# Performance work log

Hardware: AMD Instinct MI355X
Metric: run time of the kernel (lower is better)

## Reference

```python
import jax, jax.numpy as jnp
import numpy as np

MAX_ITER = 20
F_TOL = 1e-6
FREE_NUM = 64  # free_idx[1] + 1
TRUNC = (0, 512)  # truncate_idx


def setup_inputs() -> dict:
    key = jax.random.key(0)
    ks = jax.random.split(key, 8)
    bsz, in_dim, hid, out_dim, m = 1024, 512, 1024, 256, 128
    return {
        "b_primal": jax.random.normal(ks[0], (bsz, in_dim), jnp.float32),
        "W0": jax.random.normal(ks[1], (hid, in_dim), jnp.float32) / np.sqrt(in_dim).astype(np.float32),
        "b0": jnp.zeros((hid,), jnp.float32),
        "W1": jax.random.normal(ks[2], (hid, hid), jnp.float32) / np.sqrt(hid).astype(np.float32),
        "b1": jnp.zeros((hid,), jnp.float32),
        "W2": jax.random.normal(ks[3], (out_dim, hid), jnp.float32) / np.sqrt(hid).astype(np.float32),
        "b2": jnp.zeros((out_dim,), jnp.float32),
        "A": jax.random.normal(ks[4], (m, out_dim), jnp.float32) * 0.1,
        "b_vec": jax.random.normal(ks[5], (m,), jnp.float32),
        # scaled so spectral norm < 1 -> contracting fixed-point iteration
        "WzProj": jax.random.normal(ks[6], (out_dim, out_dim), jnp.float32) * 0.03,
        "WbProj": jax.random.normal(ks[7], (out_dim, m), jnp.float32) * 0.1,
    }


def reference(b_primal, W0, b0, W1, b1, W2, b2, A, b_vec, WzProj, WbProj):
    # eval-mode forward of DualNN (report_projection=True)
    x = b_primal[:, TRUNC[0]:TRUNC[1]]
    h = jax.nn.relu(x @ W0.T + b0)
    h = jax.nn.relu(h @ W1.T + b1)
    out = h @ W2.T + b2                      # [bsz, output_dim]

    bias_proj = b_vec @ WbProj.T             # [output_dim]

    def cond(state):
        _, it, res = state
        return (it <= MAX_ITER) & (res > F_TOL)

    def body(state):
        z, it, _ = state
        z = bias_proj + z @ WzProj.T         # affine projection step
        u = z[:, :FREE_NUM]
        v = jax.nn.relu(z[:, FREE_NUM:])     # clamp non-free coordinates
        z = jnp.concatenate([u, v], axis=-1)
        res = jnp.max(jnp.abs(z @ A.T - b_vec))  # inf-norm equality residual
        return z, it + 1, res

    z_star, curr_iter, _ = jax.lax.while_loop(
        cond, body, (out, jnp.int32(1), jnp.float32(jnp.inf)))
    return (z_star, out, curr_iter)
```

## Files before the change

kernel.cpp:

```cpp
#include <hip/hip_runtime.h>

typedef __attribute__((ext_vector_type(8))) __bf16 bf16x8;
typedef __attribute__((ext_vector_type(4))) float f32x4;

#define MAX_ITER_N 20
#define F_TOL_F 1e-6f
#define FREE_NUM_N 64

#define BSZ 1024
#define IN_DIM 512
#define HID 1024
#define OUT_DIM 256
#define M_CON 128

#define WS_BAR   0
#define WS_RES   8
#define WS_BP    48
#define WS_H1    304
#define WS_H2    (WS_H1 + 524288)
#define WS_W2C   (WS_H2 + 524288)
#define WS_WZG   (WS_W2C + 131072)
#define WS_AG    (WS_WZG + 32768)

__device__ __forceinline__ unsigned short f2bf(float f) {
    unsigned int u = __float_as_uint(f);
    u += 0x7fffu + ((u >> 16) & 1u);
    return (unsigned short)(u >> 16);
}

__device__ __forceinline__ uint4 cvt8(float4 a, float4 b) {
    union { unsigned short s[8]; uint4 v; } u;
    u.s[0] = f2bf(a.x); u.s[1] = f2bf(a.y); u.s[2] = f2bf(a.z); u.s[3] = f2bf(a.w);
    u.s[4] = f2bf(b.x); u.s[5] = f2bf(b.y); u.s[6] = f2bf(b.z); u.s[7] = f2bf(b.w);
    return u.v;
}

__device__ __forceinline__ void gload_lds16(const unsigned short* g, unsigned short* l) {
    __builtin_amdgcn_global_load_lds(
        (const __attribute__((address_space(1))) unsigned int*)(const void*)g,
        (__attribute__((address_space(3))) unsigned int*)(void*)l, 16, 0, 0);
}

__device__ __forceinline__ bf16x8 ldfrag(const unsigned short* p) {
    return __builtin_bit_cast(bf16x8, *(const uint4*)p);
}

__device__ __forceinline__ bf16x8 frag128(const unsigned short* lds, int row, int gc) {
    int phys = gc ^ (row & 15);
    return __builtin_bit_cast(bf16x8, *(const uint4*)(lds + row * 128 + phys * 8));
}

__device__ __forceinline__ void grid_barrier(unsigned int* bar, unsigned int nblk) {
    __syncthreads();
    if (threadIdx.x == 0) {
        unsigned int g = __hip_atomic_load(&bar[1], __ATOMIC_RELAXED, __HIP_MEMORY_SCOPE_AGENT);
        unsigned int a = __hip_atomic_fetch_add(&bar[0], 1u, __ATOMIC_ACQ_REL, __HIP_MEMORY_SCOPE_AGENT);
        if (a == nblk - 1u) {
            __hip_atomic_store(&bar[0], 0u, __ATOMIC_RELAXED, __HIP_MEMORY_SCOPE_AGENT);
            __hip_atomic_store(&bar[1], g + 1u, __ATOMIC_RELEASE, __HIP_MEMORY_SCOPE_AGENT);
        } else {
            while (__hip_atomic_load(&bar[1], __ATOMIC_ACQUIRE, __HIP_MEMORY_SCOPE_AGENT) == g)
                __builtin_amdgcn_s_sleep(2);
        }
    }
    __syncthreads();
}

template<int K, int NTN, bool AF32, bool BF32, bool RELU>
__device__ __forceinline__ void gemm32_dev(
    const void* __restrict__ Av, const void* __restrict__ Bv,
    const float* __restrict__ bias, unsigned short* __restrict__ C, int N_,
    int tile, unsigned short (*As)[32 * 128], unsigned short (*Bs)[32 * 128])
{
    constexpr int NCH = K / 128;
    const int tid = threadIdx.x;
    const int w = tid >> 6;
    const int lane = tid & 63;
    const int ln = lane & 15;
    const int q  = lane >> 4;
    const int wr = w >> 1;
    const int wc = w & 1;
    const int row0 = (tile / NTN) * 32;
    const int col0 = (tile % NTN) * 32;

    int goff[2], lgran[2], soff[2], dbase[2];
#pragma unroll
    for (int i = 0; i < 2; ++i) {
        int P = i * 256 + tid;
        int row = P >> 4, gc = P & 15;
        goff[i]  = row * K + gc * 8;
        lgran[i] = row * 128 + (gc ^ (row & 15)) * 8;
        int base = w * 128 + i * 64;
        int P2 = base + lane;
        int row2 = P2 >> 4, pgc = P2 & 15;
        soff[i]  = row2 * K + (pgc ^ (row2 & 15)) * 8;
        dbase[i] = base * 8;
    }

    const float* Af = (const float*)Av + row0 * K;
    const float* Bf = (const float*)Bv + col0 * K;
    const unsigned short* Ah = (const unsigned short*)Av + row0 * K;
    const unsigned short* Bh = (const unsigned short*)Bv + col0 * K;

    float4 fa[2][2], fb[2][2];
    if constexpr (AF32) {
#pragma unroll
        for (int i = 0; i < 2; ++i) {
            fa[i][0] = *(const float4*)(Af + goff[i]);
            fa[i][1] = *(const float4*)(Af + goff[i] + 4);
        }
#pragma unroll
        for (int i = 0; i < 2; ++i) *(uint4*)&As[0][lgran[i]] = cvt8(fa[i][0], fa[i][1]);
    } else {
#pragma unroll
        for (int i = 0; i < 2; ++i) gload_lds16(Ah + soff[i], &As[0][dbase[i]]);
    }
    if constexpr (BF32) {
#pragma unroll
        for (int i = 0; i < 2; ++i) {
            fb[i][0] = *(const float4*)(Bf + goff[i]);
            fb[i][1] = *(const float4*)(Bf + goff[i] + 4);
        }
#pragma unroll
        for (int i = 0; i < 2; ++i) *(uint4*)&Bs[0][lgran[i]] = cvt8(fb[i][0], fb[i][1]);
    } else {
#pragma unroll
        for (int i = 0; i < 2; ++i) gload_lds16(Bh + soff[i], &Bs[0][dbase[i]]);
    }

    f32x4 acc = {0.f, 0.f, 0.f, 0.f};

    for (int c = 0; c < NCH; ++c) {
        __syncthreads();
        const int nb = (c + 1) & 1;
        if (c + 1 < NCH) {
            if constexpr (AF32) {
#pragma unroll
                for (int i = 0; i < 2; ++i) {
                    fa[i][0] = *(const float4*)(Af + (c + 1) * 128 + goff[i]);
                    fa[i][1] = *(const float4*)(Af + (c + 1) * 128 + goff[i] + 4);
                }
            } else {
#pragma unroll
                for (int i = 0; i < 2; ++i)
                    gload_lds16(Ah + (c + 1) * 128 + soff[i], &As[nb][dbase[i]]);
            }
            if constexpr (BF32) {
#pragma unroll
                for (int i = 0; i < 2; ++i) {
                    fb[i][0] = *(const float4*)(Bf + (c + 1) * 128 + goff[i]);
                    fb[i][1] = *(const float4*)(Bf + (c + 1) * 128 + goff[i] + 4);
                }
            } else {
#pragma unroll
                for (int i = 0; i < 2; ++i)
                    gload_lds16(Bh + (c + 1) * 128 + soff[i], &Bs[nb][dbase[i]]);
            }
        }
        const unsigned short* Ac = As[c & 1];
        const unsigned short* Bc = Bs[c & 1];
#pragma unroll
        for (int ks = 0; ks < 4; ++ks) {
            bf16x8 af = frag128(Ac, wr * 16 + ln, ks * 4 + q);
            bf16x8 bf = frag128(Bc, wc * 16 + ln, ks * 4 + q);
            acc = __builtin_amdgcn_mfma_f32_16x16x32_bf16(af, bf, acc, 0, 0, 0);
        }
        if (c + 1 < NCH) {
            if constexpr (AF32) {
#pragma unroll
                for (int i = 0; i < 2; ++i) *(uint4*)&As[nb][lgran[i]] = cvt8(fa[i][0], fa[i][1]);
            }
            if constexpr (BF32) {
#pragma unroll
                for (int i = 0; i < 2; ++i) *(uint4*)&Bs[nb][lgran[i]] = cvt8(fb[i][0], fb[i][1]);
            }
        }
    }

    const int cc = col0 + wc * 16 + ln;
    const float bv = bias[cc];
#pragma unroll
    for (int i = 0; i < 4; ++i) {
        int r = row0 + wr * 16 + q * 4 + i;
        float v = acc[i] + bv;
        if (RELU) v = fmaxf(v, 0.0f);
        C[r * N_ + cc] = f2bf(v);
    }
}

__global__ __launch_bounds__(256, 4) void g1_k(
    const float* __restrict__ b_primal, const float* __restrict__ W0,
    const float* __restrict__ b0, float* __restrict__ ws)
{
    __shared__ __align__(16) unsigned short As[2][32 * 128];
    __shared__ __align__(16) unsigned short Bs[2][32 * 128];
    if (blockIdx.x == 0 && threadIdx.x < 40)
        ((unsigned int*)ws)[threadIdx.x] = 0u;
    unsigned short* h1c = (unsigned short*)(ws + WS_H1);
    gemm32_dev<IN_DIM, 32, true, true, true>(b_primal, W0, b0, h1c, HID,
                                             blockIdx.x, As, Bs);
}

__global__ __launch_bounds__(256, 4) void g2_k(
    const float* __restrict__ W1, const float* __restrict__ b1,
    const float* __restrict__ W2, const float* __restrict__ Wz,
    const float* __restrict__ Amat, const float* __restrict__ b_vec,
    const float* __restrict__ WbProj, float* __restrict__ ws)
{
    __shared__ __align__(16) unsigned short As[2][32 * 128];
    __shared__ __align__(16) unsigned short Bs[2][32 * 128];
    const int tid = threadIdx.x;
    if (blockIdx.x >= 1024) {
        int b = blockIdx.x - 1024;
        if (b == 352) {
            float s = 0.0f;
            const float* wrow = WbProj + tid * M_CON;
            for (int k = 0; k < M_CON; ++k) s += b_vec[k] * wrow[k];
            (ws + WS_BP)[tid] = s;
            return;
        }
        const float* src; unsigned short* dst; int off;
        if (b < 256)      { src = W2;   dst = (unsigned short*)(ws + WS_W2C); off = b; }
        else if (b < 320) { src = Wz;   dst = (unsigned short*)(ws + WS_WZG); off = b - 256; }
        else              { src = Amat; dst = (unsigned short*)(ws + WS_AG);  off = b - 320; }
        int idx = off * 1024 + tid * 4;
        float4 v = *(const float4*)(src + idx);
        ushort4 o;
        o.x = f2bf(v.x); o.y = f2bf(v.y); o.z = f2bf(v.z); o.w = f2bf(v.w);
        *(ushort4*)(dst + idx) = o;
        return;
    }
    const unsigned short* h1c = (const unsigned short*)(ws + WS_H1);
    unsigned short* h2c = (unsigned short*)(ws + WS_H2);
    gemm32_dev<HID, 32, false, true, true>(h1c, W1, b1, h2c, HID,
                                           blockIdx.x, As, Bs);
}

__global__ __launch_bounds__(256, 1) void loop_k(
    const float* __restrict__ b2, const float* __restrict__ b_vec,
    const float* __restrict__ WzProj, float* __restrict__ out,
    float* __restrict__ ws)
{
    __shared__ __align__(16) unsigned char smem[16 * 257 * 4 + 64];
    unsigned int* bar = (unsigned int*)(ws + WS_BAR);
    unsigned int* res = (unsigned int*)(ws + WS_RES);
    const float* bp = ws + WS_BP;
    const unsigned short* h2c = (const unsigned short*)(ws + WS_H2);
    const unsigned short* W2c = (const unsigned short*)(ws + WS_W2C);
    const unsigned short* WzG = (const unsigned short*)(ws + WS_WZG);
    const unsigned short* AG  = (const unsigned short*)(ws + WS_AG);
    float* outz = out + BSZ * OUT_DIM;

    const int tid  = threadIdx.x;
    const int wave = tid >> 6;
    const int lane = tid & 63;
    const int ln   = lane & 15;
    const int q    = lane >> 4;
    const int r0   = blockIdx.x * 16;

    unsigned short (*zS)[264] = (unsigned short(*)[264])smem;
    float* red = (float*)(smem + 16 * 257 * 4);

    int colg[4];
#pragma unroll
    for (int nt = 0; nt < 4; ++nt) colg[nt] = wave * 64 + nt * 16 + ln;

    {
        f32x4 acc0[4];
#pragma unroll
        for (int nt = 0; nt < 4; ++nt) acc0[nt] = (f32x4){0.f, 0.f, 0.f, 0.f};
        const unsigned short* arow = h2c + (r0 + ln) * HID + q * 8;
#pragma unroll 2
        for (int kf = 0; kf < 32; ++kf) {
            bf16x8 af = ldfrag(arow + kf * 32);
#pragma unroll
            for (int nt = 0; nt < 4; ++nt) {
                bf16x8 bf = ldfrag(W2c + colg[nt] * HID + kf * 32 + q * 8);
                acc0[nt] = __builtin_amdgcn_mfma_f32_16x16x32_bf16(af, bf, acc0[nt], 0, 0, 0);
            }
        }
        float b2v[4];
#pragma unroll
        for (int nt = 0; nt < 4; ++nt) b2v[nt] = b2[colg[nt]];
#pragma unroll
        for (int nt = 0; nt < 4; ++nt)
#pragma unroll
            for (int i = 0; i < 4; ++i) {
                float v = acc0[nt][i] + b2v[nt];
                outz[(r0 + q * 4 + i) * OUT_DIM + colg[nt]] = v;
                zS[q * 4 + i][colg[nt]] = f2bf(v);
            }
    }
    __builtin_amdgcn_sched_barrier(0);

    bf16x8 afr[2][8];
    float bvv[2];
#pragma unroll
    for (int mt = 0; mt < 2; ++mt) {
        int m = wave * 32 + mt * 16 + ln;
        bvv[mt] = b_vec[m];
#pragma unroll
        for (int ks = 0; ks < 8; ++ks)
            afr[mt][ks] = ldfrag(AG + m * OUT_DIM + ks * 32 + q * 8);
    }
    float bpv[4];
    bf16x8 wzfr[4][8];
#pragma unroll
    for (int nt = 0; nt < 4; ++nt) {
        bpv[nt] = bp[colg[nt]];
#pragma unroll
        for (int ks = 0; ks < 8; ++ks)
            wzfr[nt][ks] = ldfrag(WzG + colg[nt] * OUT_DIM + ks * 32 + q * 8);
    }
    __syncthreads();

    bf16x8 zfr[8];
#pragma unroll
    for (int ks = 0; ks < 8; ++ks)
        zfr[ks] = __builtin_bit_cast(bf16x8, *(const uint4*)&zS[ln][ks * 32 + q * 8]);

    const f32x4 zero4 = {0.f, 0.f, 0.f, 0.f};

    for (int t = 1; t <= MAX_ITER_N; ++t) {
        f32x4 acc[4];
#pragma unroll
        for (int nt = 0; nt < 4; ++nt) acc[nt] = zero4;
#pragma unroll
        for (int ks = 0; ks < 8; ++ks)
#pragma unroll
            for (int nt = 0; nt < 4; ++nt)
                acc[nt] = __builtin_amdgcn_mfma_f32_16x16x32_bf16(zfr[ks], wzfr[nt][ks], acc[nt], 0, 0, 0);
        float vals[4][4];
#pragma unroll
        for (int nt = 0; nt < 4; ++nt)
#pragma unroll
            for (int i = 0; i < 4; ++i) {
                float v = acc[nt][i] + bpv[nt];
                if (colg[nt] >= FREE_NUM_N) v = fmaxf(v, 0.0f);
                vals[nt][i] = v;
            }
        if (t == MAX_ITER_N) {
#pragma unroll
            for (int nt = 0; nt < 4; ++nt)
#pragma unroll
                for (int i = 0; i < 4; ++i)
                    out[(r0 + q * 4 + i) * OUT_DIM + colg[nt]] = vals[nt][i];
        }
        __syncthreads();
#pragma unroll
        for (int nt = 0; nt < 4; ++nt)
#pragma unroll
            for (int i = 0; i < 4; ++i)
                zS[q * 4 + i][colg[nt]] = f2bf(vals[nt][i]);
        __syncthreads();
#pragma unroll
        for (int ks = 0; ks < 8; ++ks)
            zfr[ks] = __builtin_bit_cast(bf16x8, *(const uint4*)&zS[ln][ks * 32 + q * 8]);

        f32x4 acc2[2];
        acc2[0] = zero4; acc2[1] = zero4;
#pragma unroll
        for (int ks = 0; ks < 8; ++ks)
#pragma unroll
            for (int mt = 0; mt < 2; ++mt)
                acc2[mt] = __builtin_amdgcn_mfma_f32_16x16x32_bf16(zfr[ks], afr[mt][ks], acc2[mt], 0, 0, 0);
        float lmax = 0.0f;
#pragma unroll
        for (int mt = 0; mt < 2; ++mt)
#pragma unroll
            for (int i = 0; i < 4; ++i)
                lmax = fmaxf(lmax, fabsf(acc2[mt][i] - bvv[mt]));
#pragma unroll
        for (int off = 32; off > 0; off >>= 1)
            lmax = fmaxf(lmax, __shfl_xor(lmax, off));
        if (lane == 0) red[wave] = lmax;
        __syncthreads();
        if (tid == 0) {
            float bm = fmaxf(fmaxf(red[0], red[1]), fmaxf(red[2], red[3]));
            atomicMax(res + (t - 1), __float_as_uint(bm));
        }
    }

    grid_barrier(bar, 64);

    int T = MAX_ITER_N;
    for (int t = 0; t < MAX_ITER_N; ++t) {
        float r = __uint_as_float(res[t]);
        if (!(r > F_TOL_F)) { T = t + 1; break; }
    }
    if (blockIdx.x == 0 && tid == 0)
        out[2 * BSZ * OUT_DIM] = (float)(T + 1);

    if (T < MAX_ITER_N) {
        float (*zF)[257] = (float(*)[257])smem;
        const int row = tid >> 4;
        const int c0 = (tid & 15) * 16;
        __syncthreads();
        for (int i = 0; i < 16; ++i) zF[row][c0 + i] = outz[(r0 + row) * OUT_DIM + c0 + i];
        __syncthreads();
        const int j = tid;
        const float bj = bp[j];
        for (int t = 0; t < T; ++t) {
            float acc[16] = {};
            for (int k = 0; k < OUT_DIM; ++k) {
                float w = WzProj[j * OUT_DIM + k];
#pragma unroll
                for (int r = 0; r < 16; ++r) acc[r] += zF[r][k] * w;
            }
            __syncthreads();
#pragma unroll
            for (int r = 0; r < 16; ++r) {
                float v = acc[r] + bj;
                if (j >= FREE_NUM_N) v = fmaxf(v, 0.0f);
                zF[r][j] = v;
            }
            __syncthreads();
        }
        for (int i = 0; i < 16; ++i) out[(r0 + row) * OUT_DIM + c0 + i] = zF[row][c0 + i];
    }
}

extern "C" void kernel_launch(void* const* d_in, const int* in_sizes, int n_in,
                              void* d_out, int out_size, void* d_ws, size_t ws_size,
                              hipStream_t stream) {
    const float* b_primal = (const float*)d_in[0];
    const float* W0     = (const float*)d_in[1];
    const float* b0     = (const float*)d_in[2];
    const float* W1     = (const float*)d_in[3];
    const float* b1     = (const float*)d_in[4];
    const float* W2     = (const float*)d_in[5];
    const float* b2     = (const float*)d_in[6];
    const float* Amat   = (const float*)d_in[7];
    const float* b_vec  = (const float*)d_in[8];
    const float* WzProj = (const float*)d_in[9];
    const float* WbProj = (const float*)d_in[10];
    float* out = (float*)d_out;
    float* ws  = (float*)d_ws;

    hipLaunchKernelGGL(g1_k, dim3(1024), dim3(256), 0, stream,
                       b_primal, W0, b0, ws);
    hipLaunchKernelGGL(g2_k, dim3(1024 + 353), dim3(256), 0, stream,
                       W1, b1, W2, WzProj, Amat, b_vec, WbProj, ws);
    hipLaunchKernelGGL(loop_k, dim3(64), dim3(256), 0, stream,
                       b2, b_vec, WzProj, out, ws);
}
```

Before: 152.4 us.

## Move output GEMM out of 64-block loop kernel into separate 256-block GEMM kernel

The final layer GEMM (h2 @ W2^T + b2) was previously computed inside the persistent loop kernel by only 64 blocks. It now runs as its own kernel with 256 tiles using the shared tiled GEMM routine, which converts W2 from fp32 on the fly, so the separate W2 pre-conversion blocks go away. The loop kernel now reads the fp32 output back and converts it to bf16 for its initial z. This spreads the output GEMM over more CUs, at the cost of an extra kernel launch and an extra global round trip of the output.

New measurement: 144.3 us. 5.3% less time.

```diff
diff --git a/kernel.cpp b/kernel.cpp
--- a/kernel.cpp
+++ b/kernel.cpp
@@ -18,8 +18,7 @@
 #define WS_BP    48
 #define WS_H1    304
 #define WS_H2    (WS_H1 + 524288)
-#define WS_W2C   (WS_H2 + 524288)
-#define WS_WZG   (WS_W2C + 131072)
+#define WS_WZG   (WS_H2 + 524288)
 #define WS_AG    (WS_WZG + 32768)
 
 __device__ __forceinline__ unsigned short f2bf(float f) {
@@ -66,10 +65,10 @@
     __syncthreads();
 }
 
-template<int K, int NTN, bool AF32, bool BF32, bool RELU>
+template<int K, int NTN, bool AF32, bool BF32, bool RELU, bool F32OUT>
 __device__ __forceinline__ void gemm32_dev(
     const void* __restrict__ Av, const void* __restrict__ Bv,
-    const float* __restrict__ bias, unsigned short* __restrict__ C, int N_,
+    const float* __restrict__ bias, void* __restrict__ Cv, int N_,
     int tile, unsigned short (*As)[32 * 128], unsigned short (*Bs)[32 * 128])
 {
     constexpr int NCH = K / 128;
@@ -184,7 +183,8 @@
         int r = row0 + wr * 16 + q * 4 + i;
         float v = acc[i] + bv;
         if (RELU) v = fmaxf(v, 0.0f);
-        C[r * N_ + cc] = f2bf(v);
+        if (F32OUT) ((float*)Cv)[r * N_ + cc] = v;
+        else ((unsigned short*)Cv)[r * N_ + cc] = f2bf(v);
     }
 }
 
@@ -197,22 +197,22 @@
     if (blockIdx.x == 0 && threadIdx.x < 40)
         ((unsigned int*)ws)[threadIdx.x] = 0u;
     unsigned short* h1c = (unsigned short*)(ws + WS_H1);
-    gemm32_dev<IN_DIM, 32, true, true, true>(b_primal, W0, b0, h1c, HID,
-                                             blockIdx.x, As, Bs);
+    gemm32_dev<IN_DIM, 32, true, true, true, false>(b_primal, W0, b0, h1c, HID,
+                                                    blockIdx.x, As, Bs);
 }
 
 __global__ __launch_bounds__(256, 4) void g2_k(
     const float* __restrict__ W1, const float* __restrict__ b1,
-    const float* __restrict__ W2, const float* __restrict__ Wz,
-    const float* __restrict__ Amat, const float* __restrict__ b_vec,
-    const float* __restrict__ WbProj, float* __restrict__ ws)
+    const float* __restrict__ Wz, const float* __restrict__ Amat,
+    const float* __restrict__ b_vec, const float* __restrict__ WbProj,
+    float* __restrict__ ws)
 {
     __shared__ __align__(16) unsigned short As[2][32 * 128];
     __shared__ __align__(16) unsigned short Bs[2][32 * 128];
     const int tid = threadIdx.x;
     if (blockIdx.x >= 1024) {
         int b = blockIdx.x - 1024;
-        if (b == 352) {
+        if (b == 96) {
             float s = 0.0f;
             const float* wrow = WbProj + tid * M_CON;
             for (int k = 0; k < M_CON; ++k) s += b_vec[k] * wrow[k];
@@ -220,9 +220,8 @@
             return;
         }
         const float* src; unsigned short* dst; int off;
-        if (b < 256)      { src = W2;   dst = (unsigned short*)(ws + WS_W2C); off = b; }
-        else if (b < 320) { src = Wz;   dst = (unsigned short*)(ws + WS_WZG); off = b - 256; }
-        else              { src = Amat; dst = (unsigned short*)(ws + WS_AG);  off = b - 320; }
+        if (b < 64) { src = Wz;   dst = (unsigned short*)(ws + WS_WZG); off = b; }
+        else        { src = Amat; dst = (unsigned short*)(ws + WS_AG);  off = b - 64; }
         int idx = off * 1024 + tid * 4;
         float4 v = *(const float4*)(src + idx);
         ushort4 o;
@@ -232,21 +231,30 @@
     }
     const unsigned short* h1c = (const unsigned short*)(ws + WS_H1);
     unsigned short* h2c = (unsigned short*)(ws + WS_H2);
-    gemm32_dev<HID, 32, false, true, true>(h1c, W1, b1, h2c, HID,
-                                           blockIdx.x, As, Bs);
+    gemm32_dev<HID, 32, false, true, true, false>(h1c, W1, b1, h2c, HID,
+                                                  blockIdx.x, As, Bs);
+}
+
+__global__ __launch_bounds__(256, 4) void g3_k(
+    const float* __restrict__ W2, const float* __restrict__ b2,
+    float* __restrict__ out, float* __restrict__ ws)
+{
+    __shared__ __align__(16) unsigned short As[2][32 * 128];
+    __shared__ __align__(16) unsigned short Bs[2][32 * 128];
+    const unsigned short* h2c = (const unsigned short*)(ws + WS_H2);
+    float* outz = out + BSZ * OUT_DIM;
+    gemm32_dev<HID, 8, false, true, false, true>(h2c, W2, b2, outz, OUT_DIM,
+                                                 blockIdx.x, As, Bs);
 }
 
 __global__ __launch_bounds__(256, 1) void loop_k(
-    const float* __restrict__ b2, const float* __restrict__ b_vec,
-    const float* __restrict__ WzProj, float* __restrict__ out,
-    float* __restrict__ ws)
+    const float* __restrict__ b_vec, const float* __restrict__ WzProj,
+    float* __restrict__ out, float* __restrict__ ws)
 {
     __shared__ __align__(16) unsigned char smem[16 * 257 * 4 + 64];
     unsigned int* bar = (unsigned int*)(ws + WS_BAR);
     unsigned int* res = (unsigned int*)(ws + WS_RES);
     const float* bp = ws + WS_BP;
-    const unsigned short* h2c = (const unsigned short*)(ws + WS_H2);
-    const unsigned short* W2c = (const unsigned short*)(ws + WS_W2C);
     const unsigned short* WzG = (const unsigned short*)(ws + WS_WZG);
     const unsigned short* AG  = (const unsigned short*)(ws + WS_AG);
     float* outz = out + BSZ * OUT_DIM;
@@ -261,37 +269,13 @@
     unsigned short (*zS)[264] = (unsigned short(*)[264])smem;
     float* red = (float*)(smem + 16 * 257 * 4);
 
-    int colg[4];
-#pragma unroll
-    for (int nt = 0; nt < 4; ++nt) colg[nt] = wave * 64 + nt * 16 + ln;
-
     {
-        f32x4 acc0[4];
-#pragma unroll
-        for (int nt = 0; nt < 4; ++nt) acc0[nt] = (f32x4){0.f, 0.f, 0.f, 0.f};
-        const unsigned short* arow = h2c + (r0 + ln) * HID + q * 8;
-#pragma unroll 2
-        for (int kf = 0; kf < 32; ++kf) {
-            bf16x8 af = ldfrag(arow + kf * 32);
-#pragma unroll
-            for (int nt = 0; nt < 4; ++nt) {
-                bf16x8 bf = ldfrag(W2c + colg[nt] * HID + kf * 32 + q * 8);
-                acc0[nt] = __builtin_amdgcn_mfma_f32_16x16x32_bf16(af, bf, acc0[nt], 0, 0, 0);
-            }
-        }
-        float b2v[4];
-#pragma unroll
-        for (int nt = 0; nt < 4; ++nt) b2v[nt] = b2[colg[nt]];
-#pragma unroll
-        for (int nt = 0; nt < 4; ++nt)
-#pragma unroll
-            for (int i = 0; i < 4; ++i) {
-                float v = acc0[nt][i] + b2v[nt];
-                outz[(r0 + q * 4 + i) * OUT_DIM + colg[nt]] = v;
-                zS[q * 4 + i][colg[nt]] = f2bf(v);
-            }
-    }
-    __builtin_amdgcn_sched_barrier(0);
+        int row = tid >> 4;
+        int c0  = (tid & 15) * 16;
+        const float* src = outz + (r0 + row) * OUT_DIM + c0;
+#pragma unroll
+        for (int i = 0; i < 16; ++i) zS[row][c0 + i] = f2bf(src[i]);
+    }
 
     bf16x8 afr[2][8];
     float bvv[2];
@@ -303,11 +287,13 @@
         for (int ks = 0; ks < 8; ++ks)
             afr[mt][ks] = ldfrag(AG + m * OUT_DIM + ks * 32 + q * 8);
     }
+    int colg[4];
     float bpv[4];
     bf16x8 wzfr[4][8];
 #pragma unroll
     for (int nt = 0; nt < 4; ++nt) {
-        bpv[nt] = bp[colg[nt]];
+        colg[nt] = wave * 64 + nt * 16 + ln;
+        bpv[nt]  = bp[colg[nt]];
 #pragma unroll
         for (int ks = 0; ks < 8; ++ks)
             wzfr[nt][ks] = ldfrag(WzG + colg[nt] * OUT_DIM + ks * 32 + q * 8);
@@ -439,8 +425,10 @@
 
     hipLaunchKernelGGL(g1_k, dim3(1024), dim3(256), 0, stream,
                        b_primal, W0, b0, ws);
-    hipLaunchKernelGGL(g2_k, dim3(1024 + 353), dim3(256), 0, stream,
-                       W1, b1, W2, WzProj, Amat, b_vec, WbProj, ws);
+    hipLaunchKernelGGL(g2_k, dim3(1024 + 97), dim3(256), 0, stream,
+                       W1, b1, WzProj, Amat, b_vec, WbProj, ws);
+    hipLaunchKernelGGL(g3_k, dim3(256), dim3(256), 0, stream,
+                       W2, b2, out, ws);
     hipLaunchKernelGGL(loop_k, dim3(64), dim3(256), 0, stream,
-                       b2, b_vec, WzProj, out, ws);
-}
+                       b_vec, WzProj, out, ws);
+}
```
